# Optimization experiments

Hardware: AMD Instinct MI355X
Metric: run time of the kernel (lower is better)

Reference implementation:

```python
import jax, jax.numpy as jnp
import numpy as np

N_E = 8192
SPLIT = (512, 512)
BETA = 0.25
ENTROPY_RATIO = 0.1
TEMPERATURE = 0.01


def _l2norm(x):
    return x / jnp.linalg.norm(x, axis=-1, keepdims=True)


def _pairwise_sq_dist(zf, emb):
    # ||z||^2 + ||e||^2 - 2 z @ e^T   -> [N, n_e]
    return (jnp.sum(zf ** 2, axis=1, keepdims=True)
            + jnp.sum(emb ** 2, axis=1)
            - 2.0 * jnp.einsum('bd,nd->bn', zf, emb))


def _entropy_loss(affinity):
    flat = affinity / TEMPERATURE                      # [N, n_e]
    probs = jax.nn.softmax(flat, axis=-1)
    log_probs = jax.nn.log_softmax(flat + 1e-5, axis=-1)
    avg_probs = jnp.mean(probs, axis=0)                # [n_e]
    avg_entropy = -jnp.sum(avg_probs * jnp.log(avg_probs + 1e-5))
    sample_entropy = -jnp.mean(jnp.sum(probs * log_probs, axis=-1))
    return sample_entropy - avg_entropy


def setup_inputs() -> dict:
    key = jax.random.key(0)
    k1, k2, k3 = jax.random.split(key, 3)
    z = jax.random.normal(k1, (8192, 1024), dtype=jnp.float32)
    lim = 1.0 / N_E
    emb_text = jax.random.uniform(k2, (N_E, SPLIT[0]), minval=-lim, maxval=lim, dtype=jnp.float32)
    emb_graph = jax.random.uniform(k3, (N_E, SPLIT[1]), minval=-lim, maxval=lim, dtype=jnp.float32)
    # l2_norm=True: codebook weights are normalized at init
    emb_text = _l2norm(emb_text)
    emb_graph = _l2norm(emb_graph)
    return {"z": z, "emb_text": emb_text, "emb_graph": emb_graph}


def reference(z, emb_text, emb_graph):
    st = SPLIT[0]
    z_text, z_graph = z[:, :st], z[:, st:]

    # l2_norm path: normalize inputs and codebooks
    zt = _l2norm(z_text)                               # [N, d_t]
    zg = _l2norm(z_graph)                              # [N, d_g]
    et = _l2norm(emb_text)                             # [n_e, d_t]
    eg = _l2norm(emb_graph)                            # [n_e, d_g]
    z_norm = jnp.concatenate([zt, zg], axis=-1)        # [N, e_dim]

    d_text = _pairwise_sq_dist(zt, et)                 # [N, n_e]
    d_graph = _pairwise_sq_dist(zg, eg)                # [N, n_e]
    text_d_norm = jnp.mean(jnp.sum(d_text ** 2, axis=-1))
    graph_d_norm = jnp.mean(jnp.sum(d_graph ** 2, axis=-1))

    d = d_text + 1.0 * d_graph
    min_encoding_indices = jnp.argmin(d, axis=1)       # [N]

    all_embedding = jnp.concatenate([et, eg], axis=-1) # [n_e, e_dim]
    z_q = all_embedding[min_encoding_indices]          # [N, e_dim]
    z_q_text = et[min_encoding_indices]
    z_q_graph = eg[min_encoding_indices]

    sg = jax.lax.stop_gradient
    vq_loss = jnp.mean((z_q - sg(z_norm)) ** 2)
    commit_loss = BETA * jnp.mean((sg(z_q) - z_norm) ** 2)
    entropy_loss = ENTROPY_RATIO * _entropy_loss(-d)

    z_q_out = z_norm + sg(z_q - z_norm)                # straight-through
    return (z_q_out, vq_loss, commit_loss, entropy_loss,
            text_d_norm, graph_d_norm, z_q_text, z_q_graph,
            min_encoding_indices)
```

## Files before the change

kernel.cpp:

```cpp
#include <hip/hip_runtime.h>
#include <cmath>

using f32x4 = __attribute__((ext_vector_type(4))) float;
using f16x8 = __attribute__((ext_vector_type(8))) _Float16;

#define SCL_H  256.0f
#define INV_HH (1.0f/65536.0f)

#define WS_ZH   ((size_t)0)
#define WS_ZL   ((size_t)4194304)
#define WS_EH   ((size_t)8388608)
#define WS_EL   ((size_t)12582912)
#define WS_Z2T  ((size_t)16777216)
#define WS_Z2G  ((size_t)16785408)
#define WS_E2T  ((size_t)16793600)
#define WS_E2G  ((size_t)16801792)
#define WS_PM   ((size_t)16809984)
#define WS_PZ   ((size_t)17858560)
#define WS_PS1  ((size_t)18907136)
#define WS_PDT  ((size_t)19955712)
#define WS_PDG  ((size_t)21004288)
#define WS_PD1  ((size_t)22052864)
#define WS_PD2  ((size_t)23101440)
#define WS_PI1  ((size_t)24150016)
#define WS_PI2  ((size_t)25198592)
#define WS_PSC  ((size_t)26247168)
#define WS_LSE  ((size_t)27295744)
#define WS_IDX  ((size_t)27303936)
#define WS_RENT ((size_t)27312128)
#define WS_RDT  ((size_t)27320320)
#define WS_RDG  ((size_t)27328512)
#define WS_GVQ  ((size_t)27336704)
#define WS_AVG4 ((size_t)27344896)
#define WS_QM   ((size_t)27418624)
#define WS_STORE_END ((size_t)60973056)

#define O_VQ  ((size_t)8388608)
#define O_CM  ((size_t)8388609)
#define O_ENT ((size_t)8388610)
#define O_TD  ((size_t)8388611)
#define O_GD  ((size_t)8388612)
#define O_ZT  ((size_t)8388613)
#define O_ZG  ((size_t)12582917)
#define O_IX  ((size_t)16777221)

__device__ __forceinline__ size_t tiled_off(int row, int chunk) {
    return (((size_t)(row >> 7) * 32 + (chunk >> 2)) * 4 + (size_t)(chunk & 3)) * 1024
           + (size_t)(row & 127) * 8;
}

__device__ __forceinline__ void gload16(const void* g, void* l) {
    __builtin_amdgcn_global_load_lds(
        (const __attribute__((address_space(1))) unsigned int*)g,
        (__attribute__((address_space(3))) unsigned int*)l, 16, 0, 0);
}

__device__ __forceinline__ f32x4 mfma16(f16x8 a, f16x8 b, f32x4 c) {
    return __builtin_amdgcn_mfma_f32_16x16x32_f16(a, b, c, 0, 0, 0);
}

__device__ __forceinline__ unsigned short f2bf(float x) {
    unsigned int u = __float_as_uint(x);
    return (unsigned short)((u + 0x7fffu + ((u >> 16) & 1u)) >> 16);
}
__device__ __forceinline__ float bf2f(unsigned short u) {
    return __uint_as_float(((unsigned int)u) << 16);
}

__device__ __forceinline__ bool dless(float a, int ia, float b, int ib) {
    return a < b || (a == b && ia < ib);
}
__device__ __forceinline__ void top2_point(float& d1, int& i1, float& d2, int& i2,
                                           float d, int j) {
    if (dless(d, j, d1, i1)) { d2 = d1; i2 = i1; d1 = d; i1 = j; }
    else if (dless(d, j, d2, i2)) { d2 = d; i2 = j; }
}
__device__ __forceinline__ void top2_merge(float& d1, int& i1, float& d2, int& i2,
                                           float od1, int oi1, float od2, int oi2) {
    if (dless(od1, oi1, d1, i1)) {
        float nd2; int ni2;
        if (dless(d1, i1, od2, oi2)) { nd2 = d1; ni2 = i1; } else { nd2 = od2; ni2 = oi2; }
        d1 = od1; i1 = oi1; d2 = nd2; i2 = ni2;
    } else if (dless(od1, oi1, d2, i2)) {
        d2 = od1; i2 = oi1;
    }
}

__global__ __launch_bounds__(256) void k_zero(float* __restrict__ p, int n) {
    int i = blockIdx.x * 256 + threadIdx.x;
    if (i < n) p[i] = 0.0f;
}

__global__ __launch_bounds__(1024) void k_norm_z(const float* __restrict__ z,
        _Float16* __restrict__ zh, _Float16* __restrict__ zl,
        float* __restrict__ z2t, float* __restrict__ z2g) {
    int t = threadIdx.x;
    int r8 = t & 7, ck = t >> 3;
    int row = blockIdx.x * 8 + r8;
    const float* src = z + (size_t)row * 1024 + (size_t)ck * 8;
    float4 v0 = *(const float4*)src;
    float4 v1 = *(const float4*)(src + 4);
    float v[8] = {v0.x,v0.y,v0.z,v0.w,v1.x,v1.y,v1.z,v1.w};
    float ss = 0.f;
#pragma unroll
    for (int e = 0; e < 8; ++e) ss += v[e]*v[e];
    __shared__ float red[8*132];
    int ri = r8*132 + ck;
    red[ri] = ss; __syncthreads();
    for (int s = 32; s > 0; s >>= 1) { if ((ck & 63) < s) red[ri] += red[ri+s]; __syncthreads(); }
    float nrm = sqrtf(red[r8*132 + (ck & 64)]);
    float nv[8]; float s2 = 0.f;
#pragma unroll
    for (int e = 0; e < 8; ++e) { nv[e] = v[e]/nrm; s2 += nv[e]*nv[e]; }
    __syncthreads();
    red[ri] = s2; __syncthreads();
    for (int s = 32; s > 0; s >>= 1) { if ((ck & 63) < s) red[ri] += red[ri+s]; __syncthreads(); }
    if ((ck & 63) == 0) { if (ck & 64) z2g[row] = red[ri]; else z2t[row] = red[ri]; }
    f16x8 h8, l8;
#pragma unroll
    for (int e = 0; e < 8; ++e) {
        float xs = nv[e]*SCL_H;
        _Float16 h = (_Float16)xs; h8[e] = h;
        l8[e] = (_Float16)((xs - (float)h) * 4096.0f);
    }
    size_t off = tiled_off(row, ck);
    *(f16x8*)(zh + off) = h8;
    *(f16x8*)(zl + off) = l8;
}

__global__ __launch_bounds__(1024) void k_norm_e(const float* __restrict__ et, const float* __restrict__ eg,
        _Float16* __restrict__ eh, _Float16* __restrict__ el,
        float* __restrict__ e2t, float* __restrict__ e2g) {
    int t = threadIdx.x;
    int r8 = t & 7, ck = t >> 3;
    int row = blockIdx.x * 8 + r8;
    const float* src = (ck < 64) ? (et + (size_t)row * 512 + (size_t)ck * 8)
                                 : (eg + (size_t)row * 512 + (size_t)(ck - 64) * 8);
    float4 v0 = *(const float4*)src;
    float4 v1 = *(const float4*)(src + 4);
    float v[8] = {v0.x,v0.y,v0.z,v0.w,v1.x,v1.y,v1.z,v1.w};
    float ss = 0.f;
#pragma unroll
    for (int e = 0; e < 8; ++e) ss += v[e]*v[e];
    __shared__ float red[8*132];
    int ri = r8*132 + ck;
    red[ri] = ss; __syncthreads();
    for (int s = 32; s > 0; s >>= 1) { if ((ck & 63) < s) red[ri] += red[ri+s]; __syncthreads(); }
    float nrm = sqrtf(red[r8*132 + (ck & 64)]);
    float nv[8]; float s2 = 0.f;
#pragma unroll
    for (int e = 0; e < 8; ++e) { nv[e] = v[e]/nrm; s2 += nv[e]*nv[e]; }
    __syncthreads();
    red[ri] = s2; __syncthreads();
    for (int s = 32; s > 0; s >>= 1) { if ((ck & 63) < s) red[ri] += red[ri+s]; __syncthreads(); }
    if ((ck & 63) == 0) { if (ck & 64) e2g[row] = red[ri]; else e2t[row] = red[ri]; }
    f16x8 h8, l8;
#pragma unroll
    for (int e = 0; e < 8; ++e) {
        float xs = nv[e]*SCL_H;
        _Float16 h = (_Float16)xs; h8[e] = h;
        l8[e] = (_Float16)((xs - (float)h) * 4096.0f);
    }
    size_t off = tiled_off(row, ck);
    *(f16x8*)(eh + off) = h8;
    *(f16x8*)(el + off) = l8;
}

template<int PASS, bool STOREQ>
__global__ __launch_bounds__(256, 3) void k_gemm(
    const _Float16* __restrict__ zht, const _Float16* __restrict__ eht,
    const float* __restrict__ z2t, const float* __restrict__ z2g,
    const float* __restrict__ e2t, const float* __restrict__ e2g,
    float* __restrict__ pm, float* __restrict__ pz, float* __restrict__ ps1,
    float* __restrict__ pdt, float* __restrict__ pdg,
    float* __restrict__ pd1, float* __restrict__ pd2,
    int* __restrict__ pi1, int* __restrict__ pi2,
    unsigned short* __restrict__ qm,
    const float* __restrict__ lse, float* __restrict__ avgp)
{
    const int bid = blockIdx.x;
    const int xcd = bid & 7, local = bid >> 3;
    const int nj = local >> 3;
    const int bi = xcd * 8 + (local & 7);

    const int t = threadIdx.x;
    const int lane = t & 63, wid = t >> 6;
    const int wave_r = wid >> 1, wave_c = wid & 1;
    const int jf = lane & 15, g = lane >> 4;

    __shared__ __align__(16) char smem[35328];
    _Float16* lA = (_Float16*)smem;
    _Float16* lB = (_Float16*)(smem + 16384);
    unsigned short* sQ = (unsigned short*)smem;
    float (*sM)[2]  = (float(*)[2])(smem + 24576);
    float (*sDt)[2] = (float(*)[2])(smem + 25600);
    float (*sDg)[2] = (float(*)[2])(smem + 26624);
    float (*sZ)[2]  = (float(*)[2])(smem + 27648);
    float (*sS1)[2] = (float(*)[2])(smem + 28672);
    float (*sD1)[2] = (float(*)[2])(smem + 29696);
    float (*sD2)[2] = (float(*)[2])(smem + 30720);
    int   (*sI1)[2] = (int(*)[2])(smem + 31744);
    int   (*sI2)[2] = (int(*)[2])(smem + 32768);
    float* sMf  = (float*)(smem + 33792);
    float* scol = (float*)(smem + 34304);

    if (PASS == 2 && t < 64) scol[t] = 0.f;

    f32x4 acct[4][2] = {};
    f32x4 accg[4][2] = {};

    const _Float16* pa  = zht + (size_t)bi * 131072;
    const _Float16* pbv = eht + (size_t)(nj >> 1) * 131072 + (size_t)(nj & 1) * 512;

#define STAGE(KT2) { \
        size_t kofs = (size_t)(KT2) * 8192; \
        gload16(pa + kofs + (size_t)t * 8,         lA + t * 8); \
        gload16(pa + kofs + (size_t)(256 + t) * 8, lA + (256 + t) * 8); \
        gload16(pa + kofs + (size_t)(512 + t) * 8, lA + (512 + t) * 8); \
        gload16(pa + kofs + (size_t)(768 + t) * 8, lA + (768 + t) * 8); \
        { int li = t;       gload16(pbv + kofs + (size_t)(li >> 6) * 1024 + (size_t)(li & 63) * 8, lB + li * 8); } \
        { int li = 256 + t; gload16(pbv + kofs + (size_t)(li >> 6) * 1024 + (size_t)(li & 63) * 8, lB + li * 8); } }

    for (int kt2 = 0; kt2 < 16; ++kt2) {
        STAGE(kt2)
        asm volatile("s_waitcnt vmcnt(0)" ::: "memory");
        __syncthreads();
        f16x8 a0[4], a1[4], b0[2], b1[2];
#pragma unroll
        for (int fr = 0; fr < 4; ++fr) {
            int ro = (wave_r * 64 + fr * 16 + jf) * 8;
            a0[fr] = *(const f16x8*)&lA[g * 1024 + ro];
            a1[fr] = *(const f16x8*)&lA[4096 + g * 1024 + ro];
        }
#pragma unroll
        for (int fc = 0; fc < 2; ++fc) {
            int ro = (wave_c * 32 + fc * 16 + jf) * 8;
            b0[fc] = *(const f16x8*)&lB[g * 512 + ro];
            b1[fc] = *(const f16x8*)&lB[2048 + g * 512 + ro];
        }
        if (kt2 < 8) {
#pragma unroll
            for (int fr = 0; fr < 4; ++fr)
#pragma unroll
            for (int fc = 0; fc < 2; ++fc) {
                acct[fr][fc] = mfma16(a0[fr], b0[fc], acct[fr][fc]);
                acct[fr][fc] = mfma16(a1[fr], b1[fc], acct[fr][fc]);
            }
        } else {
#pragma unroll
            for (int fr = 0; fr < 4; ++fr)
#pragma unroll
            for (int fc = 0; fc < 2; ++fc) {
                accg[fr][fc] = mfma16(a0[fr], b0[fc], accg[fr][fc]);
                accg[fr][fc] = mfma16(a1[fr], b1[fc], accg[fr][fc]);
            }
        }
        __syncthreads();
    }
#undef STAGE

    const int colbase = nj * 64 + wave_c * 32;
    float e2tc[2], e2gc[2];
#pragma unroll
    for (int fc = 0; fc < 2; ++fc) {
        e2tc[fc] = e2t[colbase + fc * 16 + jf];
        e2gc[fc] = e2g[colbase + fc * 16 + jf];
    }

    if constexpr (PASS == 1) {
#pragma unroll
        for (int fr = 0; fr < 4; ++fr) {
#pragma unroll
            for (int reg = 0; reg < 4; ++reg) {
                int rl = wave_r * 64 + fr * 16 + g * 4 + reg;
                int i  = bi * 128 + rl;
                float z2ti = z2t[i], z2gi = z2g[i];
                float mrow = -3.0e38f, dt2 = 0.f, dg2 = 0.f;
                float d1 = 3.0e38f, d2 = 3.0e38f;
                int i1 = 0x7fffffff, i2 = 0x7fffffff;
#pragma unroll
                for (int fc = 0; fc < 2; ++fc) {
                    float ht = acct[fr][fc][reg], hg = accg[fr][fc][reg];
                    float dta = z2ti + e2tc[fc] - ht * (2.0f * INV_HH);
                    float dga = z2gi + e2gc[fc] - hg * (2.0f * INV_HH);
                    float d   = dta + dga;
                    float lv  = -100.0f * d;
                    acct[fr][fc][reg] = lv;
                    dt2 += dta * dta; dg2 += dga * dga;
                    int j = colbase + fc * 16 + jf;
                    top2_point(d1, i1, d2, i2, d, j);
                    mrow = fmaxf(mrow, lv);
                }
#pragma unroll
                for (int s = 1; s < 16; s <<= 1) {
                    mrow = fmaxf(mrow, __shfl_xor(mrow, s));
                    dt2 += __shfl_xor(dt2, s);
                    dg2 += __shfl_xor(dg2, s);
                    float od1 = __shfl_xor(d1, s); int oi1 = __shfl_xor(i1, s);
                    float od2 = __shfl_xor(d2, s); int oi2 = __shfl_xor(i2, s);
                    top2_merge(d1, i1, d2, i2, od1, oi1, od2, oi2);
                }
                if (jf == 0) {
                    sM[rl][wave_c] = mrow; sDt[rl][wave_c] = dt2; sDg[rl][wave_c] = dg2;
                    sD1[rl][wave_c] = d1; sI1[rl][wave_c] = i1;
                    sD2[rl][wave_c] = d2; sI2[rl][wave_c] = i2;
                }
            }
        }
        __syncthreads();
        if (t < 128) sMf[t] = fmaxf(sM[t][0], sM[t][1]);
        __syncthreads();
#pragma unroll
        for (int fr = 0; fr < 4; ++fr) {
#pragma unroll
            for (int reg = 0; reg < 4; ++reg) {
                int rl = wave_r * 64 + fr * 16 + g * 4 + reg;
                float M = sMf[rl];
                float Z = 0.f, S1 = 0.f;
#pragma unroll
                for (int fc = 0; fc < 2; ++fc) {
                    float lv = acct[fr][fc][reg];
                    float e  = expf(lv - M);
                    Z += e; S1 += e * lv;
                    if constexpr (STOREQ) sQ[rl * 64 + wave_c * 32 + fc * 16 + jf] = f2bf(e);
                }
#pragma unroll
                for (int s = 1; s < 16; s <<= 1) {
                    Z  += __shfl_xor(Z, s);
                    S1 += __shfl_xor(S1, s);
                }
                if (jf == 0) { sZ[rl][wave_c] = Z; sS1[rl][wave_c] = S1; }
            }
        }
        __syncthreads();
        if (t < 128) {
            float M = sMf[t];
            float Z = sZ[t][0] + sZ[t][1];
            float S1 = sS1[t][0] + sS1[t][1];
            float dt2 = sDt[t][0] + sDt[t][1];
            float dg2 = sDg[t][0] + sDg[t][1];
            float d1 = sD1[t][0], d2 = sD2[t][0];
            int i1 = sI1[t][0], i2 = sI2[t][0];
            top2_merge(d1, i1, d2, i2, sD1[t][1], sI1[t][1], sD2[t][1], sI2[t][1]);
            size_t pb = (size_t)nj * 8192 + (bi * 128 + t);
            pm[pb] = M; pz[pb] = Z; ps1[pb] = S1;
            pdt[pb] = dt2; pdg[pb] = dg2;
            pd1[pb] = d1; pd2[pb] = d2; pi1[pb] = i1; pi2[pb] = i2;
        }
        if constexpr (STOREQ) {
            const uint4* s4 = (const uint4*)sQ;
#pragma unroll
            for (int it = 0; it < 4; ++it) {
                int f = it * 256 + t;
                int row = f >> 3, seg = f & 7;
                uint4 q = s4[f];
                *(uint4*)(qm + (size_t)(bi * 128 + row) * 8192 + nj * 64 + seg * 8) = q;
            }
        }
    } else {
        float cs0 = 0.f, cs1 = 0.f;
#pragma unroll
        for (int fr = 0; fr < 4; ++fr) {
#pragma unroll
            for (int reg = 0; reg < 4; ++reg) {
                int rl = wave_r * 64 + fr * 16 + g * 4 + reg;
                int i  = bi * 128 + rl;
                float z2ti = z2t[i], z2gi = z2g[i];
                float lsei = lse[i];
#pragma unroll
                for (int fc = 0; fc < 2; ++fc) {
                    float ht = acct[fr][fc][reg], hg = accg[fr][fc][reg];
                    float d = (z2ti + z2gi) + (e2tc[fc] + e2gc[fc])
                            - 2.0f * INV_HH * (ht + hg);
                    float lv = -100.0f * d;
                    float p = expf(lv - lsei);
                    if (fc == 0) cs0 += p; else cs1 += p;
                }
            }
        }
        cs0 += __shfl_xor(cs0, 16); cs0 += __shfl_xor(cs0, 32);
        cs1 += __shfl_xor(cs1, 16); cs1 += __shfl_xor(cs1, 32);
        if (g == 0) {
            atomicAdd(&scol[wave_c * 32 + jf], cs0);
            atomicAdd(&scol[wave_c * 32 + 16 + jf], cs1);
        }
        __syncthreads();
        if (t < 64) atomicAdd(&avgp[nj * 64 + t], scol[t]);
    }
}

__global__ __launch_bounds__(256) void k_rowreduce(
    const float* __restrict__ pm, const float* __restrict__ pz, const float* __restrict__ ps1,
    const float* __restrict__ pdt, const float* __restrict__ pdg,
    float* __restrict__ pscale, float* __restrict__ lse,
    float* __restrict__ rent, float* __restrict__ rdt, float* __restrict__ rdg)
{
    int row = blockIdx.x * 256 + threadIdx.x;
    float m = -3.0e38f, Z = 0.f, S1 = 0.f, dt2 = 0.f, dg2 = 0.f;
#pragma unroll 4
    for (int nj = 0; nj < 128; ++nj) {
        size_t pb = (size_t)nj * 8192 + row;
        float m0 = pm[pb];
        if (m0 > m) {
            float sc = expf(m - m0);
            Z *= sc; S1 *= sc; m = m0;
        }
        float sc0 = expf(m0 - m);
        Z  += pz[pb] * sc0;
        S1 += ps1[pb] * sc0;
        dt2 += pdt[pb]; dg2 += pdg[pb];
    }
    float lseb = m + logf(Z);
    lse[row] = lseb;
    rent[row] = lseb - S1 / Z;
    rdt[row] = dt2; rdg[row] = dg2;
#pragma unroll 4
    for (int nj = 0; nj < 128; ++nj) {
        size_t pb = (size_t)nj * 8192 + row;
        pscale[pb] = expf(pm[pb] - lseb);
    }
}

__global__ __launch_bounds__(256) void k_refine(
    const float* __restrict__ pd1, const float* __restrict__ pd2,
    const int* __restrict__ pi1, const int* __restrict__ pi2,
    const _Float16* __restrict__ zh, const _Float16* __restrict__ zl,
    const _Float16* __restrict__ eh, const _Float16* __restrict__ el,
    const float* __restrict__ z2t, const float* __restrict__ z2g,
    const float* __restrict__ e2t, const float* __restrict__ e2g,
    int* __restrict__ idxi, float* __restrict__ out)
{
    int row = blockIdx.x * 4 + (threadIdx.x >> 6);
    int l = threadIdx.x & 63;
    size_t b0 = (size_t)l * 8192 + row, b1 = (size_t)(l + 64) * 8192 + row;
    float cd[4]; int ci[4];
    cd[0] = pd1[b0]; ci[0] = pi1[b0];
    cd[1] = pd1[b1]; ci[1] = pi1[b1];
    cd[2] = pd2[b0]; ci[2] = pi2[b0];
    cd[3] = pd2[b1]; ci[3] = pi2[b1];
    float M = fminf(fminf(cd[0], cd[1]), fminf(cd[2], cd[3]));
#pragma unroll
    for (int s = 1; s < 64; s <<= 1) M = fminf(M, __shfl_xor(M, s));
    const float eps = 4.0e-3f;
    unsigned long long mk[4];
#pragma unroll
    for (int k = 0; k < 4; ++k) mk[k] = __ballot(cd[k] <= M + eps);

    float zv[16];
    {
        size_t o0 = tiled_off(row, 2 * l), o1 = tiled_off(row, 2 * l + 1);
        f16x8 h0 = *(const f16x8*)(zh + o0), l0 = *(const f16x8*)(zl + o0);
        f16x8 h1 = *(const f16x8*)(zh + o1), l1 = *(const f16x8*)(zl + o1);
#pragma unroll
        for (int e = 0; e < 8; ++e) {
            zv[e]     = (float)h0[e] * (1.0f/256.0f) + (float)l0[e] * (1.0f/1048576.0f);
            zv[8 + e] = (float)h1[e] * (1.0f/256.0f) + (float)l1[e] * (1.0f/1048576.0f);
        }
    }
    float zz = z2t[row] + z2g[row];
    float bd = 3.0e38f; int bj = 0x7fffffff;
#pragma unroll 1
    for (int k = 0; k < 4; ++k) {
        while (mk[k]) {
            int s = (int)__ffsll(mk[k]) - 1; mk[k] &= mk[k] - 1;
            int cand = __shfl(ci[k], s);
            size_t o0 = tiled_off(cand, 2 * l), o1 = tiled_off(cand, 2 * l + 1);
            f16x8 h0 = *(const f16x8*)(eh + o0), l0 = *(const f16x8*)(el + o0);
            f16x8 h1 = *(const f16x8*)(eh + o1), l1 = *(const f16x8*)(el + o1);
            float dot = 0.f;
#pragma unroll
            for (int e = 0; e < 8; ++e) {
                float ev0 = (float)h0[e] * (1.0f/256.0f) + (float)l0[e] * (1.0f/1048576.0f);
                float ev1 = (float)h1[e] * (1.0f/256.0f) + (float)l1[e] * (1.0f/1048576.0f);
                dot += zv[e] * ev0 + zv[8 + e] * ev1;
            }
#pragma unroll
            for (int s2 = 1; s2 < 64; s2 <<= 1) dot += __shfl_xor(dot, s2);
            float d = zz + e2t[cand] + e2g[cand] - 2.0f * dot;
            if (d < bd || (d == bd && cand < bj)) { bd = d; bj = cand; }
        }
    }
    if (l == 0) { idxi[row] = bj; out[O_IX + row] = (float)bj; }
}

__global__ __launch_bounds__(256) void k_colsum(const unsigned short* __restrict__ qm,
                                                const float* __restrict__ pscale,
                                                float* __restrict__ avg4) {
    int cc = blockIdx.x, rb = blockIdx.y, t = threadIdx.x;
    int cp = t & 31, rg = t >> 5;
    float a0 = 0.f, a1 = 0.f;
    const unsigned short* qb = qm + (size_t)cc * 64 + (size_t)cp * 2;
    const float* psb = pscale + (size_t)cc * 8192;
#pragma unroll 4
    for (int rr = rg; rr < 1024; rr += 8) {
        int r = rb * 1024 + rr;
        float s = psb[r];
        unsigned int q = *(const unsigned int*)(qb + (size_t)r * 8192);
        a0 += bf2f((unsigned short)(q & 0xffffu)) * s;
        a1 += bf2f((unsigned short)(q >> 16)) * s;
    }
    __shared__ float red[512];
    red[rg * 64 + cp * 2] = a0; red[rg * 64 + cp * 2 + 1] = a1;
    __syncthreads();
    if (rg == 0) {
        float s0 = 0.f, s1 = 0.f;
#pragma unroll
        for (int k = 0; k < 8; ++k) { s0 += red[k * 64 + cp * 2]; s1 += red[k * 64 + cp * 2 + 1]; }
        avg4[(size_t)rb * 8192 + cc * 64 + cp * 2]     = s0;
        avg4[(size_t)rb * 8192 + cc * 64 + cp * 2 + 1] = s1;
    }
}

__global__ __launch_bounds__(1024) void k_gather(
    const _Float16* __restrict__ zh, const _Float16* __restrict__ zl,
    const _Float16* __restrict__ eh, const _Float16* __restrict__ el,
    const int* __restrict__ idxi, float* __restrict__ out, float* __restrict__ gvq)
{
    int t = threadIdx.x;
    int r8 = t & 7, ck = t >> 3;
    int b = blockIdx.x * 8 + r8;
    int idx = idxi[b];
    size_t zo = tiled_off(b, ck), eo = tiled_off(idx, ck);
    f16x8 zh8 = *(const f16x8*)(zh + zo);
    f16x8 zl8 = *(const f16x8*)(zl + zo);
    f16x8 eh8 = *(const f16x8*)(eh + eo);
    f16x8 el8 = *(const f16x8*)(el + eo);
    float ss = 0.f; float oz[8], zq[8];
#pragma unroll
    for (int e = 0; e < 8; ++e) {
        float zn = ((float)zh8[e] + (float)zl8[e] * (1.0f / 4096.0f)) * (1.0f / SCL_H);
        float eq = ((float)eh8[e] + (float)el8[e] * (1.0f / 4096.0f)) * (1.0f / SCL_H);
        float df = eq - zn;
        zq[e] = eq; oz[e] = zn + df; ss += df * df;
    }
    float* dst = out + (size_t)b * 1024 + (size_t)ck * 8;
    *(float4*)dst       = make_float4(oz[0], oz[1], oz[2], oz[3]);
    *(float4*)(dst + 4) = make_float4(oz[4], oz[5], oz[6], oz[7]);
    float* tg = (ck < 64) ? (out + O_ZT + (size_t)b * 512 + (size_t)ck * 8)
                          : (out + O_ZG + (size_t)b * 512 + (size_t)(ck - 64) * 8);
    *(float4*)tg       = make_float4(zq[0], zq[1], zq[2], zq[3]);
    *(float4*)(tg + 4) = make_float4(zq[4], zq[5], zq[6], zq[7]);
    __shared__ float red[8*132];
    int ri = r8 * 132 + ck;
    red[ri] = ss; __syncthreads();
    for (int s = 64; s > 0; s >>= 1) { if (ck < s) red[ri] += red[ri + s]; __syncthreads(); }
    if (ck == 0) gvq[b] = red[ri];
}

__global__ __launch_bounds__(256) void k_finalize(const float* __restrict__ avg4,
        const float* __restrict__ rent, const float* __restrict__ rdt,
        const float* __restrict__ rdg, const float* __restrict__ gvq,
        float* __restrict__ out) {
    int t = threadIdx.x;
    float ent = 0.f, se = 0.f, dt = 0.f, dg = 0.f, vq = 0.f;
    for (int n = t; n < 8192; n += 256) {
        float a = 0.f;
#pragma unroll
        for (int k = 0; k < 8; ++k) a += avg4[(size_t)k * 8192 + n];
        a *= (1.0f / 8192.0f);
        ent -= a * logf(a + 1e-5f);
        se += rent[n]; dt += rdt[n]; dg += rdg[n]; vq += gvq[n];
    }
    __shared__ float red[256];
#define RED(x) { red[t] = x; __syncthreads(); \
    for (int s = 128; s > 0; s >>= 1) { if (t < s) red[t] += red[t + s]; __syncthreads(); } \
    x = red[0]; __syncthreads(); }
    RED(ent) RED(se) RED(dt) RED(dg) RED(vq)
#undef RED
    if (t == 0) {
        float vqm = vq * (1.0f / 8388608.0f);
        out[O_VQ]  = vqm;
        out[O_CM]  = 0.25f * vqm;
        out[O_ENT] = 0.1f * (se * (1.0f / 8192.0f) - ent);
        out[O_TD]  = dt * (1.0f / 8192.0f);
        out[O_GD]  = dg * (1.0f / 8192.0f);
    }
}

extern "C" void kernel_launch(void* const* d_in, const int* in_sizes, int n_in,
                              void* d_out, int out_size, void* d_ws, size_t ws_size,
                              hipStream_t stream) {
    const float* z  = (const float*)d_in[0];
    const float* et = (const float*)d_in[1];
    const float* eg = (const float*)d_in[2];
    float* out = (float*)d_out;
    float* ws  = (float*)d_ws;

    _Float16* zh = (_Float16*)(ws + WS_ZH);
    _Float16* zl = (_Float16*)(ws + WS_ZL);
    _Float16* eh = (_Float16*)(ws + WS_EH);
    _Float16* el = (_Float16*)(ws + WS_EL);
    float* z2t = ws + WS_Z2T;
    float* z2g = ws + WS_Z2G;
    float* e2t = ws + WS_E2T;
    float* e2g = ws + WS_E2G;
    float* pm  = ws + WS_PM;
    float* pz  = ws + WS_PZ;
    float* ps1 = ws + WS_PS1;
    float* pdt = ws + WS_PDT;
    float* pdg = ws + WS_PDG;
    float* pd1 = ws + WS_PD1;
    float* pd2 = ws + WS_PD2;
    int*   pi1 = (int*)(ws + WS_PI1);
    int*   pi2 = (int*)(ws + WS_PI2);
    float* psc = ws + WS_PSC;
    float* lsep = ws + WS_LSE;
    int*   idxi = (int*)(ws + WS_IDX);
    float* rent = ws + WS_RENT;
    float* rdt  = ws + WS_RDT;
    float* rdg  = ws + WS_RDG;
    float* gvq  = ws + WS_GVQ;
    float* avg4 = ws + WS_AVG4;
    unsigned short* qm = (unsigned short*)(ws + WS_QM);

    bool storeq = (ws_size >= WS_STORE_END * sizeof(float));

    k_norm_z<<<1024, 1024, 0, stream>>>(z, zh, zl, z2t, z2g);
    k_norm_e<<<1024, 1024, 0, stream>>>(et, eg, eh, el, e2t, e2g);

    if (storeq) {
        k_gemm<1, true><<<8192, 256, 0, stream>>>(zh, eh, z2t, z2g, e2t, e2g,
                                                  pm, pz, ps1, pdt, pdg,
                                                  pd1, pd2, pi1, pi2, qm, lsep, avg4);
    } else {
        k_gemm<1, false><<<8192, 256, 0, stream>>>(zh, eh, z2t, z2g, e2t, e2g,
                                                   pm, pz, ps1, pdt, pdg,
                                                   pd1, pd2, pi1, pi2, qm, lsep, avg4);
    }
    k_rowreduce<<<32, 256, 0, stream>>>(pm, pz, ps1, pdt, pdg,
                                        psc, lsep, rent, rdt, rdg);
    k_refine<<<2048, 256, 0, stream>>>(pd1, pd2, pi1, pi2, zh, zl, eh, el,
                                       z2t, z2g, e2t, e2g, idxi, out);
    if (storeq) {
        k_colsum<<<dim3(128, 8), 256, 0, stream>>>(qm, psc, avg4);
    } else {
        k_zero<<<256, 256, 0, stream>>>(avg4, 65536);
        k_gemm<2, false><<<8192, 256, 0, stream>>>(zh, eh, z2t, z2g, e2t, e2g,
                                                   pm, pz, ps1, pdt, pdg,
                                                   pd1, pd2, pi1, pi2, qm, lsep, avg4);
    }
    k_gather<<<1024, 1024, 0, stream>>>(zh, zl, eh, el, idxi, out, gvq);
    k_finalize<<<1, 256, 0, stream>>>(avg4, rent, rdt, rdg, gvq, out);
}
```

Measured before the change: 713.0 us.

## Double-buffer GEMM LDS staging and fuse softmax scale into colsum

```diff
diff --git a/kernel.cpp b/kernel.cpp
--- a/kernel.cpp
+++ b/kernel.cpp
@@ -24,16 +24,15 @@
 #define WS_PD2  ((size_t)23101440)
 #define WS_PI1  ((size_t)24150016)
 #define WS_PI2  ((size_t)25198592)
-#define WS_PSC  ((size_t)26247168)
-#define WS_LSE  ((size_t)27295744)
-#define WS_IDX  ((size_t)27303936)
-#define WS_RENT ((size_t)27312128)
-#define WS_RDT  ((size_t)27320320)
-#define WS_RDG  ((size_t)27328512)
-#define WS_GVQ  ((size_t)27336704)
-#define WS_AVG4 ((size_t)27344896)
-#define WS_QM   ((size_t)27418624)
-#define WS_STORE_END ((size_t)60973056)
+#define WS_LSE  ((size_t)26247168)
+#define WS_IDX  ((size_t)26255360)
+#define WS_RENT ((size_t)26263552)
+#define WS_RDT  ((size_t)26271744)
+#define WS_RDG  ((size_t)26279936)
+#define WS_GVQ  ((size_t)26288128)
+#define WS_AVG4 ((size_t)26296320)
+#define WS_QM   ((size_t)26370048)
+#define WS_STORE_END ((size_t)59924480)
 
 #define O_VQ  ((size_t)8388608)
 #define O_CM  ((size_t)8388609)
@@ -188,23 +187,19 @@
     const int wave_r = wid >> 1, wave_c = wid & 1;
     const int jf = lane & 15, g = lane >> 4;
 
-    __shared__ __align__(16) char smem[35328];
-    _Float16* lA = (_Float16*)smem;
-    _Float16* lB = (_Float16*)(smem + 16384);
+    __shared__ __align__(16) char smem[49152];
     unsigned short* sQ = (unsigned short*)smem;
-    float (*sM)[2]  = (float(*)[2])(smem + 24576);
-    float (*sDt)[2] = (float(*)[2])(smem + 25600);
-    float (*sDg)[2] = (float(*)[2])(smem + 26624);
-    float (*sZ)[2]  = (float(*)[2])(smem + 27648);
-    float (*sS1)[2] = (float(*)[2])(smem + 28672);
-    float (*sD1)[2] = (float(*)[2])(smem + 29696);
-    float (*sD2)[2] = (float(*)[2])(smem + 30720);
-    int   (*sI1)[2] = (int(*)[2])(smem + 31744);
-    int   (*sI2)[2] = (int(*)[2])(smem + 32768);
-    float* sMf  = (float*)(smem + 33792);
-    float* scol = (float*)(smem + 34304);
-
-    if (PASS == 2 && t < 64) scol[t] = 0.f;
+    float (*sM)[2]  = (float(*)[2])(smem + 16384);
+    float (*sDt)[2] = (float(*)[2])(smem + 17408);
+    float (*sDg)[2] = (float(*)[2])(smem + 18432);
+    float (*sZ)[2]  = (float(*)[2])(smem + 19456);
+    float (*sS1)[2] = (float(*)[2])(smem + 20480);
+    float (*sD1)[2] = (float(*)[2])(smem + 21504);
+    float (*sD2)[2] = (float(*)[2])(smem + 22528);
+    int   (*sI1)[2] = (int(*)[2])(smem + 23552);
+    int   (*sI2)[2] = (int(*)[2])(smem + 24576);
+    float* sMf  = (float*)(smem + 25600);
+    float* scol = (float*)(smem + 26112);
 
     f32x4 acct[4][2] = {};
     f32x4 accg[4][2] = {};
@@ -212,19 +207,29 @@
     const _Float16* pa  = zht + (size_t)bi * 131072;
     const _Float16* pbv = eht + (size_t)(nj >> 1) * 131072 + (size_t)(nj & 1) * 512;
 
-#define STAGE(KT2) { \
+#define STAGE(KT2, B) { \
         size_t kofs = (size_t)(KT2) * 8192; \
-        gload16(pa + kofs + (size_t)t * 8,         lA + t * 8); \
-        gload16(pa + kofs + (size_t)(256 + t) * 8, lA + (256 + t) * 8); \
-        gload16(pa + kofs + (size_t)(512 + t) * 8, lA + (512 + t) * 8); \
-        gload16(pa + kofs + (size_t)(768 + t) * 8, lA + (768 + t) * 8); \
-        { int li = t;       gload16(pbv + kofs + (size_t)(li >> 6) * 1024 + (size_t)(li & 63) * 8, lB + li * 8); } \
-        { int li = 256 + t; gload16(pbv + kofs + (size_t)(li >> 6) * 1024 + (size_t)(li & 63) * 8, lB + li * 8); } }
-
+        _Float16* la = (_Float16*)(smem + (B) * 24576); \
+        _Float16* lb = (_Float16*)(smem + (B) * 24576 + 16384); \
+        gload16(pa + kofs + (size_t)t * 8,         la + t * 8); \
+        gload16(pa + kofs + (size_t)(256 + t) * 8, la + (256 + t) * 8); \
+        gload16(pa + kofs + (size_t)(512 + t) * 8, la + (512 + t) * 8); \
+        gload16(pa + kofs + (size_t)(768 + t) * 8, la + (768 + t) * 8); \
+        { int li = t;       gload16(pbv + kofs + (size_t)(li >> 6) * 1024 + (size_t)(li & 63) * 8, lb + li * 8); } \
+        { int li = 256 + t; gload16(pbv + kofs + (size_t)(li >> 6) * 1024 + (size_t)(li & 63) * 8, lb + li * 8); } }
+
+    STAGE(0, 0)
+    int buf = 0;
     for (int kt2 = 0; kt2 < 16; ++kt2) {
-        STAGE(kt2)
-        asm volatile("s_waitcnt vmcnt(0)" ::: "memory");
+        if (kt2 < 15) {
+            STAGE(kt2 + 1, buf ^ 1)
+            asm volatile("s_waitcnt vmcnt(6)" ::: "memory");
+        } else {
+            asm volatile("s_waitcnt vmcnt(0)" ::: "memory");
+        }
         __syncthreads();
+        const _Float16* lA = (const _Float16*)(smem + buf * 24576);
+        const _Float16* lB = (const _Float16*)(smem + buf * 24576 + 16384);
         f16x8 a0[4], a1[4], b0[2], b1[2];
 #pragma unroll
         for (int fr = 0; fr < 4; ++fr) {
@@ -256,8 +261,11 @@
             }
         }
         __syncthreads();
+        buf ^= 1;
     }
 #undef STAGE
+
+    if (PASS == 2 && t < 64) scol[t] = 0.f;
 
     const int colbase = nj * 64 + wave_c * 32;
     float e2tc[2], e2gc[2];
@@ -392,7 +400,7 @@
 __global__ __launch_bounds__(256) void k_rowreduce(
     const float* __restrict__ pm, const float* __restrict__ pz, const float* __restrict__ ps1,
     const float* __restrict__ pdt, const float* __restrict__ pdg,
-    float* __restrict__ pscale, float* __restrict__ lse,
+    float* __restrict__ lse,
     float* __restrict__ rent, float* __restrict__ rdt, float* __restrict__ rdg)
 {
     int row = blockIdx.x * 256 + threadIdx.x;
@@ -414,11 +422,6 @@
     lse[row] = lseb;
     rent[row] = lseb - S1 / Z;
     rdt[row] = dt2; rdg[row] = dg2;
-#pragma unroll 4
-    for (int nj = 0; nj < 128; ++nj) {
-        size_t pb = (size_t)nj * 8192 + row;
-        pscale[pb] = expf(pm[pb] - lseb);
-    }
 }
 
 __global__ __launch_bounds__(256) void k_refine(
@@ -484,17 +487,18 @@
 }
 
 __global__ __launch_bounds__(256) void k_colsum(const unsigned short* __restrict__ qm,
-                                                const float* __restrict__ pscale,
+                                                const float* __restrict__ pm,
+                                                const float* __restrict__ lse,
                                                 float* __restrict__ avg4) {
     int cc = blockIdx.x, rb = blockIdx.y, t = threadIdx.x;
     int cp = t & 31, rg = t >> 5;
     float a0 = 0.f, a1 = 0.f;
     const unsigned short* qb = qm + (size_t)cc * 64 + (size_t)cp * 2;
-    const float* psb = pscale + (size_t)cc * 8192;
+    const float* pmb = pm + (size_t)cc * 8192;
 #pragma unroll 4
     for (int rr = rg; rr < 1024; rr += 8) {
         int r = rb * 1024 + rr;
-        float s = psb[r];
+        float s = expf(pmb[r] - lse[r]);
         unsigned int q = *(const unsigned int*)(qb + (size_t)r * 8192);
         a0 += bf2f((unsigned short)(q & 0xffffu)) * s;
         a1 += bf2f((unsigned short)(q >> 16)) * s;
@@ -603,7 +607,6 @@
     float* pd2 = ws + WS_PD2;
     int*   pi1 = (int*)(ws + WS_PI1);
     int*   pi2 = (int*)(ws + WS_PI2);
-    float* psc = ws + WS_PSC;
     float* lsep = ws + WS_LSE;
     int*   idxi = (int*)(ws + WS_IDX);
     float* rent = ws + WS_RENT;
@@ -628,11 +631,11 @@
                                                    pd1, pd2, pi1, pi2, qm, lsep, avg4);
     }
     k_rowreduce<<<32, 256, 0, stream>>>(pm, pz, ps1, pdt, pdg,
-                                        psc, lsep, rent, rdt, rdg);
+                                        lsep, rent, rdt, rdg);
     k_refine<<<2048, 256, 0, stream>>>(pd1, pd2, pi1, pi2, zh, zl, eh, el,
                                        z2t, z2g, e2t, e2g, idxi, out);
     if (storeq) {
-        k_colsum<<<dim3(128, 8), 256, 0, stream>>>(qm, psc, avg4);
+        k_colsum<<<dim3(128, 8), 256, 0, stream>>>(qm, pm, lsep, avg4);
     } else {
         k_zero<<<256, 256, 0, stream>>>(avg4, 65536);
         k_gemm<2, false><<<8192, 256, 0, stream>>>(zh, eh, z2t, z2g, e2t, e2g,
```

After: 703.8 us. Within noise of the previous version (-1.3%).
